# Kernel tuning notes

Hardware: AMD Instinct MI355X
Metric: run time of the kernel (lower is better)

Reference implementation:

```python
import jax, jax.numpy as jnp
import numpy as np

# Static architecture constants (match init_kwargs)
N, M, DIM = 2048, 4096, 256
KS = (0.9, 0.8, 0.7)
HEADS, BOT_HEADS = 4, 2
NEG_SLOPE = 0.2  # PyG GATConv default leaky-relu slope


def _p(key, shape, scale):
    return (scale * jax.random.normal(key, shape, dtype=jnp.float32))


def setup_inputs() -> dict:
    key = jax.random.key(0)
    ks = jax.random.split(key, 16)
    # Symmetric positive connectivity matrix (fMRI-like), fully dense
    R = jax.random.uniform(ks[0], (N, N), dtype=jnp.float32)
    A = 0.5 * (R + R.T)
    X = jax.random.normal(ks[1], (N, DIM), dtype=jnp.float32)
    s = 1.0 / np.sqrt(DIM).astype(np.float32)
    C, Cb = DIM // HEADS, DIM // BOT_HEADS
    inp = {
        'A': A, 'X': X,
        'W_down': _p(ks[2], (3, DIM, DIM), s),
        'as_down': _p(ks[3], (3, HEADS, C), s),
        'ad_down': _p(ks[4], (3, HEADS, C), s),
        'b_down': jnp.zeros((3, DIM), jnp.float32),
        'W_up': _p(ks[5], (3, DIM, DIM), s),
        'as_up': _p(ks[6], (3, HEADS, C), s),
        'ad_up': _p(ks[7], (3, HEADS, C), s),
        'b_up': jnp.zeros((3, DIM), jnp.float32),
        'W_bot': _p(ks[8], (DIM, DIM), s),
        'as_bot': _p(ks[9], (BOT_HEADS, Cb), s),
        'ad_bot': _p(ks[10], (BOT_HEADS, Cb), s),
        'b_bot': jnp.zeros((DIM,), jnp.float32),
        'W_pool': _p(ks[11], (3, DIM), s),
        'b_pool': jnp.zeros((3,), jnp.float32),
        'W_ups': _p(ks[12], (M, N), 1.0 / np.sqrt(N).astype(np.float32)),
        'b_ups': jnp.zeros((M,), jnp.float32),
    }
    return inp


def _sym_norm(A):
    # A_tilde = A + I ; D^{-1/2} A_tilde D^{-1/2} as elementwise broadcast
    A = A + jnp.eye(A.shape[0], dtype=A.dtype)
    d = A.sum(axis=1) + 1e-5
    di = d ** -0.5
    return di[:, None] * A * di[None, :]


def _gat(A, X, W, a_src, a_dst, b):
    # Dense-masked GATConv (concat=True, eval mode => no dropout).
    # Edge j->i exists iff A[j, i] > 0 (dense_to_sparse row=src, col=tgt).
    n = X.shape[0]
    H, C = a_src.shape
    x = (X @ W).reshape(n, H, C)                       # [n, H, C]
    s = jnp.einsum('nhc,hc->nh', x, a_src)             # source logit term
    t = jnp.einsum('nhc,hc->nh', x, a_dst)             # target logit term
    logits = jax.nn.leaky_relu(t[:, None, :] + s[None, :, :], NEG_SLOPE)  # [i, j, h]
    mask = (A.T > 0)[:, :, None]
    attn = jax.nn.softmax(jnp.where(mask, logits, -jnp.inf), axis=1)
    out = jnp.einsum('ijh,jhc->ihc', attn, x).reshape(n, H * C) + b
    return jax.nn.relu(out)


def reference(A, X, W_down, as_down, ad_down, b_down,
              W_up, as_up, ad_up, b_up,
              W_bot, as_bot, ad_bot, b_bot,
              W_pool, b_pool, W_ups, b_ups):
    A = _sym_norm(A)
    A_hist, idx_hist = [], []
    # Encoder: GAT -> top-k pool (gather rows/cols)
    for i in range(3):
        X = _gat(A, X, W_down[i], as_down[i], ad_down[i], b_down[i])
        A_hist.append(A)
        scores = jax.nn.sigmoid(X @ W_pool[i] + b_pool[i])
        k = max(2, int(KS[i] * A.shape[0]))            # static sizes
        vals, idx = jax.lax.top_k(scores, k)
        X = X[idx] * vals[:, None]
        A = A[idx][:, idx]
        idx_hist.append(idx)
    X = _gat(A, X, W_bot, as_bot, ad_bot, b_bot)
    # Decoder: scatter-unpool -> GAT -> adjacency reconstruction
    for i in range(3):
        u = 2 - i
        A, idx = A_hist[u], idx_hist[u]
        Xn = jnp.zeros((A.shape[0], X.shape[1]), X.dtype).at[idx].set(X)
        X = _gat(A, Xn, W_up[i], as_up[i], ad_up[i], b_up[i])
    # Upsampler: Linear(n->m) on X^T, then A_up = relu(Xu Xu^T)
    X_up = W_ups @ X + b_ups[:, None]                  # [M, DIM]
    A_up = jax.nn.relu(X_up @ X_up.T)                  # [M, M]
    return A_up
```

## Files before the change

kernel.cpp:

```cpp
#include <hip/hip_runtime.h>
#include <math.h>

#define NEG 0.2f
#define NMAX 2048
#define CHUNK 64
#define NCHMAX 32

__device__ __forceinline__ float lrelu(float v) { return v > 0.f ? v : NEG * v; }
__device__ __forceinline__ unsigned fenc(float v) {
    unsigned u = __float_as_uint(v);
    return (u & 0x80000000u) ? ~u : (u | 0x80000000u);
}
__device__ __forceinline__ float fdec(unsigned u) {
    return (u & 0x80000000u) ? __uint_as_float(u ^ 0x80000000u) : __uint_as_float(~u);
}

__global__ __launch_bounds__(256) void gemm_ks(const float* __restrict__ A,
                                               const float* __restrict__ B,
                                               float* __restrict__ C, int M, int N, int K) {
    __shared__ float As[16][68];
    __shared__ float Bs[16][68];
    const int tid = threadIdx.x;
    const int m0 = blockIdx.x * 64, n0 = blockIdx.y * 64;
    const int kchunk = K / gridDim.z;
    const int kbeg = blockIdx.z * kchunk, kend = kbeg + kchunk;
    const int tm = tid >> 4, tn = tid & 15;
    const int lr = tid >> 2, lc4 = (tid & 3) * 4;
    const int br = tid >> 4, bc4 = (tid & 15) * 4;
    float acc[4][4] = {{0.f}};
    for (int k0 = kbeg; k0 < kend; k0 += 16) {
        {
            int m = m0 + lr;
            float4 v = make_float4(0.f, 0.f, 0.f, 0.f);
            if (m < M) v = *(const float4*)(A + (size_t)m * K + k0 + lc4);
            As[lc4 + 0][lr] = v.x; As[lc4 + 1][lr] = v.y;
            As[lc4 + 2][lr] = v.z; As[lc4 + 3][lr] = v.w;
        }
        {
            float4 v = *(const float4*)(B + (size_t)(k0 + br) * N + n0 + bc4);
            *(float4*)&Bs[br][bc4] = v;
        }
        __syncthreads();
#pragma unroll
        for (int kk = 0; kk < 16; ++kk) {
            float a[4], b[4];
            *(float4*)a = *(const float4*)&As[kk][tm * 4];
            *(float4*)b = *(const float4*)&Bs[kk][tn * 4];
#pragma unroll
            for (int x = 0; x < 4; ++x)
#pragma unroll
                for (int y = 0; y < 4; ++y) acc[x][y] = fmaf(a[x], b[y], acc[x][y]);
        }
        __syncthreads();
    }
#pragma unroll
    for (int x = 0; x < 4; ++x) {
        int m = m0 + tm * 4 + x;
        if (m >= M) continue;
        float* dst = C + (size_t)m * N + n0 + tn * 4;
#pragma unroll
        for (int y = 0; y < 4; ++y) atomicAdd(dst + y, acc[x][y]);
    }
}

__global__ __launch_bounds__(256) void st_kernel(const float* __restrict__ xw,
                                                 const float* __restrict__ asrc,
                                                 const float* __restrict__ adst,
                                                 float* __restrict__ S, float* __restrict__ T,
                                                 unsigned* __restrict__ SMX,
                                                 int n, int Hh, int Cc) {
    int gid = blockIdx.x * 256 + threadIdx.x;
    int i = gid / Hh, h = gid - i * Hh;
    float s = -INFINITY;
    if (i < n) {
        const float* xr = xw + (size_t)i * 256 + h * Cc;
        const float* pa = asrc + h * Cc;
        const float* pd = adst + h * Cc;
        float sv = 0.f, tv = 0.f;
        for (int c = 0; c < Cc; c += 4) {
            float4 xv = *(const float4*)(xr + c);
            float4 av = *(const float4*)(pa + c);
            float4 dv = *(const float4*)(pd + c);
            sv += xv.x * av.x + xv.y * av.y + xv.z * av.z + xv.w * av.w;
            tv += xv.x * dv.x + xv.y * dv.y + xv.z * dv.z + xv.w * dv.w;
        }
        S[(size_t)i * Hh + h] = sv;
        T[(size_t)i * Hh + h] = tv;
        s = sv;
    }
    for (int off = Hh; off < 64; off <<= 1) s = fmaxf(s, __shfl_xor(s, off));
    int lane = threadIdx.x & 63;
    if (lane < Hh && s > -INFINITY) atomicMax(SMX + lane, fenc(s));
}

__global__ __launch_bounds__(256) void rank_k(const float* __restrict__ S,
                                              float* __restrict__ SS, int* __restrict__ PERM,
                                              int n, int Hh) {
    __shared__ float s[NMAX];
    int h = blockIdx.y;
    for (int j = threadIdx.x; j < n; j += 256) s[j] = S[(size_t)j * Hh + h];
    __syncthreads();
    int i = blockIdx.x * 256 + threadIdx.x;
    if (i >= n) return;
    float v = s[i];
    int cnt = 0, j = 0;
    for (; j + 4 <= n; j += 4) {
        float4 sv = *(const float4*)&s[j];
        cnt += (sv.x > v) || (sv.x == v && (j + 0) < i);
        cnt += (sv.y > v) || (sv.y == v && (j + 1) < i);
        cnt += (sv.z > v) || (sv.z == v && (j + 2) < i);
        cnt += (sv.w > v) || (sv.w == v && (j + 3) < i);
    }
    for (; j < n; ++j) {
        float sj = s[j];
        cnt += (sj > v) || (sj == v && j < i);
    }
    SS[h * NMAX + cnt] = v;
    PERM[h * NMAX + cnt] = i;
}

__global__ void scanA(const float* __restrict__ XW, const float* __restrict__ SS,
                      const int* __restrict__ PERM, const unsigned* __restrict__ SMX,
                      float* __restrict__ P1L, float* __restrict__ S2L,
                      float* __restrict__ Z1L, float* __restrict__ Z2L,
                      float* __restrict__ TOT1, float* __restrict__ TOT2,
                      float* __restrict__ ZT1, float* __restrict__ ZT2, int n) {
    const int C = blockDim.x, c = threadIdx.x;
    const int h = blockIdx.x, dir = blockIdx.y, ch = blockIdx.z;
    const float smax = fdec(SMX[h]);
    const int r0 = ch * CHUNK, r1 = min(n, r0 + CHUNK);
    float carry = 0.f, zc = 0.f;
    if (dir == 0) {
#pragma unroll 4
        for (int r = r0; r < r1; ++r) {
            float ssv = SS[h * NMAX + r];
            int j = PERM[h * NMAX + r];
            float xv = XW[(size_t)j * 256 + h * C + c];
            P1L[((size_t)h * NMAX + r) * C + c] = carry;
            if (c == 0) Z1L[h * NMAX + r] = zc;
            float w = expf(ssv - smax);
            carry = fmaf(w, xv, carry);
            zc += w;
        }
        TOT1[((size_t)h * NCHMAX + ch) * C + c] = carry;
        if (c == 0) ZT1[h * NCHMAX + ch] = zc;
    } else {
#pragma unroll 4
        for (int r = r1 - 1; r >= r0; --r) {
            float ssv = SS[h * NMAX + r];
            int j = PERM[h * NMAX + r];
            float xv = XW[(size_t)j * 256 + h * C + c];
            float w = expf(NEG * (ssv - smax));
            carry = fmaf(w, xv, carry);
            zc += w;
            S2L[((size_t)h * NMAX + r) * C + c] = carry;
            if (c == 0) Z2L[h * NMAX + r] = zc;
        }
        TOT2[((size_t)h * NCHMAX + ch) * C + c] = carry;
        if (c == 0) ZT2[h * NCHMAX + ch] = zc;
    }
}

__global__ void scanB(const float* __restrict__ TOT1, const float* __restrict__ TOT2,
                      const float* __restrict__ ZT1, const float* __restrict__ ZT2,
                      float* __restrict__ OFF1, float* __restrict__ OFFB,
                      float* __restrict__ ZO1, float* __restrict__ ZOB, int nch) {
    const int C = blockDim.x, c = threadIdx.x;
    const int h = blockIdx.x, dir = blockIdx.y;
    if (dir == 0) {
        float off = 0.f, zo = 0.f;
        for (int ch = 0; ch <= nch; ++ch) {
            OFF1[((size_t)h * (NCHMAX + 1) + ch) * C + c] = off;
            if (c == 0) ZO1[h * (NCHMAX + 1) + ch] = zo;
            if (ch < nch) {
                off += TOT1[((size_t)h * NCHMAX + ch) * C + c];
                if (c == 0) {}
                zo += ZT1[h * NCHMAX + ch];
            }
        }
    } else {
        float off = 0.f, zo = 0.f;
        for (int ch = nch - 1; ch >= 0; --ch) {
            OFFB[((size_t)h * (NCHMAX + 1) + ch) * C + c] = off;
            if (c == 0) ZOB[h * (NCHMAX + 1) + ch] = zo;
            off += TOT2[((size_t)h * NCHMAX + ch) * C + c];
            zo += ZT2[h * NCHMAX + ch];
        }
    }
}

__global__ __launch_bounds__(256) void combine_k(
    const float* __restrict__ P1L, const float* __restrict__ S2L,
    const float* __restrict__ Z1L, const float* __restrict__ Z2L,
    const float* __restrict__ OFF1, const float* __restrict__ OFFB,
    const float* __restrict__ ZO1, const float* __restrict__ ZOB,
    const float* __restrict__ SS, const float* __restrict__ T,
    const unsigned* __restrict__ SMX, const float* __restrict__ bias,
    const float* __restrict__ Wp, const float* __restrict__ bp,
    float* __restrict__ Xout, float* __restrict__ SC, int n, int Hh) {
    const int i = blockIdx.x, t = threadIdx.x;
    const int C = 256 / Hh;
    const int nch = (n + CHUNK - 1) / CHUNK;
    __shared__ int qs[4];
    __shared__ float f1s[4], f2s[4], invs[4];
    __shared__ float red[256];
    if (t < Hh) {
        int h = t;
        float tv = T[(size_t)i * Hh + h];
        float smax = fdec(SMX[h]);
        float u = tv + smax, m = lrelu(u);
        float f1 = expf(u - m), f2 = expf(NEG * u - m);
        float thr = -tv;
        int lo = 0, hi = n;
        while (lo < hi) {
            int mid = (lo + hi) >> 1;
            if (SS[h * NMAX + mid] > thr) lo = mid + 1; else hi = mid;
        }
        int q = lo;
        float z1, z2;
        if (q == n) {
            z1 = ZO1[h * (NCHMAX + 1) + nch];
            z2 = 0.f;
        } else {
            int ch = q / CHUNK;
            z1 = ZO1[h * (NCHMAX + 1) + ch] + Z1L[h * NMAX + q];
            z2 = ZOB[h * (NCHMAX + 1) + ch] + Z2L[h * NMAX + q];
        }
        qs[h] = q; f1s[h] = f1; f2s[h] = f2;
        invs[h] = 1.f / (f1 * z1 + f2 * z2);
    }
    __syncthreads();
    const int h = t / C, c = t - h * C;
    const int q = qs[h];
    const float f1 = f1s[h], f2 = f2s[h], inv = invs[h];
    float p1, s2;
    if (q == n) {
        p1 = OFF1[((size_t)h * (NCHMAX + 1) + nch) * C + c];
        s2 = 0.f;
    } else {
        int ch = q / CHUNK;
        p1 = OFF1[((size_t)h * (NCHMAX + 1) + ch) * C + c] + P1L[((size_t)h * NMAX + q) * C + c];
        s2 = OFFB[((size_t)h * (NCHMAX + 1) + ch) * C + c] + S2L[((size_t)h * NMAX + q) * C + c];
    }
    float out = fmaf(f1, p1, f2 * s2) * inv + bias[t];
    out = fmaxf(out, 0.f);
    Xout[(size_t)i * 256 + t] = out;
    if (Wp) {
        red[t] = out * Wp[t];
        __syncthreads();
        for (int s = 128; s > 0; s >>= 1) {
            if (t < s) red[t] += red[t + s];
            __syncthreads();
        }
        if (t == 0) SC[i] = 1.f / (1.f + expf(-(red[0] + bp[0])));
    }
}

__global__ __launch_bounds__(256) void topk_k(const float* __restrict__ SC,
                                              int* __restrict__ IDX, int n, int k) {
    __shared__ float s[NMAX];
    for (int j = threadIdx.x; j < n; j += 256) s[j] = SC[j];
    __syncthreads();
    int i = blockIdx.x * 256 + threadIdx.x;
    if (i >= n) return;
    float v = s[i];
    int cnt = 0, j = 0;
    for (; j + 4 <= n; j += 4) {
        float4 sv = *(const float4*)&s[j];
        cnt += (sv.x > v) || (sv.x == v && (j + 0) < i);
        cnt += (sv.y > v) || (sv.y == v && (j + 1) < i);
        cnt += (sv.z > v) || (sv.z == v && (j + 2) < i);
        cnt += (sv.w > v) || (sv.w == v && (j + 3) < i);
    }
    for (; j < n; ++j) {
        float sj = s[j];
        cnt += (sj > v) || (sj == v && j < i);
    }
    if (cnt < k) IDX[cnt] = i;
}

__global__ __launch_bounds__(256) void gather_k(const float* __restrict__ Xin,
                                                const float* __restrict__ SC,
                                                const int* __restrict__ IDX,
                                                float* __restrict__ Xout, int k) {
    int gid = blockIdx.x * 256 + threadIdx.x;
    if (gid >= k * 64) return;
    int r = gid >> 6, d4 = (gid & 63) * 4;
    int src = IDX[r];
    float val = SC[src];
    float4 x = *(const float4*)(Xin + (size_t)src * 256 + d4);
    x.x *= val; x.y *= val; x.z *= val; x.w *= val;
    *(float4*)(Xout + (size_t)r * 256 + d4) = x;
}

__global__ __launch_bounds__(256) void scatter_k(const float* __restrict__ Xin,
                                                 const int* __restrict__ IDX,
                                                 float* __restrict__ Xout, int k) {
    int gid = blockIdx.x * 256 + threadIdx.x;
    if (gid >= k * 64) return;
    int r = gid >> 6, d4 = (gid & 63) * 4;
    int dst = IDX[r];
    *(float4*)(Xout + (size_t)dst * 256 + d4) = *(const float4*)(Xin + (size_t)r * 256 + d4);
}

__global__ __launch_bounds__(256) void ttr_sym(const float* __restrict__ A,
                                               const float* __restrict__ bias,
                                               float* __restrict__ C, int M, int K) {
    if (blockIdx.y < blockIdx.x) return;
    __shared__ float As[8][132];
    __shared__ float Bs[8][132];
    const int tid = threadIdx.x;
    const int m0 = blockIdx.x * 128, n0 = blockIdx.y * 128;
    const int lr = tid >> 1, lc4 = (tid & 1) * 4;
    const int tm = tid >> 4, tn = tid & 15;
    const float abias = bias[m0 + lr], bbias = bias[n0 + lr];
    float acc[8][8] = {{0.f}};
    for (int k0 = 0; k0 < K; k0 += 8) {
        float4 va = *(const float4*)(A + (size_t)(m0 + lr) * K + k0 + lc4);
        float4 vb = *(const float4*)(A + (size_t)(n0 + lr) * K + k0 + lc4);
        va.x += abias; va.y += abias; va.z += abias; va.w += abias;
        vb.x += bbias; vb.y += bbias; vb.z += bbias; vb.w += bbias;
        As[lc4 + 0][lr] = va.x; As[lc4 + 1][lr] = va.y;
        As[lc4 + 2][lr] = va.z; As[lc4 + 3][lr] = va.w;
        Bs[lc4 + 0][lr] = vb.x; Bs[lc4 + 1][lr] = vb.y;
        Bs[lc4 + 2][lr] = vb.z; Bs[lc4 + 3][lr] = vb.w;
        __syncthreads();
#pragma unroll
        for (int kk = 0; kk < 8; ++kk) {
            float a[8], b[8];
            *(float4*)&a[0] = *(const float4*)&As[kk][tm * 8];
            *(float4*)&a[4] = *(const float4*)&As[kk][tm * 8 + 4];
            *(float4*)&b[0] = *(const float4*)&Bs[kk][tn * 8];
            *(float4*)&b[4] = *(const float4*)&Bs[kk][tn * 8 + 4];
#pragma unroll
            for (int x = 0; x < 8; ++x)
#pragma unroll
                for (int y = 0; y < 8; ++y) acc[x][y] = fmaf(a[x], b[y], acc[x][y]);
        }
        __syncthreads();
    }
#pragma unroll
    for (int x = 0; x < 8; ++x)
#pragma unroll
        for (int y = 0; y < 8; ++y) acc[x][y] = fmaxf(acc[x][y], 0.f);
#pragma unroll
    for (int x = 0; x < 8; ++x) {
        float* dst = C + (size_t)(m0 + tm * 8 + x) * M + n0 + tn * 8;
        *(float4*)dst = make_float4(acc[x][0], acc[x][1], acc[x][2], acc[x][3]);
        *(float4*)(dst + 4) = make_float4(acc[x][4], acc[x][5], acc[x][6], acc[x][7]);
    }
    if (blockIdx.x != blockIdx.y) {
#pragma unroll
        for (int y = 0; y < 8; ++y) {
            float* dst = C + (size_t)(n0 + tn * 8 + y) * M + m0 + tm * 8;
            *(float4*)dst = make_float4(acc[0][y], acc[1][y], acc[2][y], acc[3][y]);
            *(float4*)(dst + 4) = make_float4(acc[4][y], acc[5][y], acc[6][y], acc[7][y]);
        }
    }
}

extern "C" void kernel_launch(void* const* d_in, const int* in_sizes, int n_in,
                              void* d_out, int out_size, void* d_ws, size_t ws_size,
                              hipStream_t stream) {
    const float* X0      = (const float*)d_in[1];
    const float* W_down  = (const float*)d_in[2];
    const float* as_down = (const float*)d_in[3];
    const float* ad_down = (const float*)d_in[4];
    const float* b_down  = (const float*)d_in[5];
    const float* W_up    = (const float*)d_in[6];
    const float* as_up   = (const float*)d_in[7];
    const float* ad_up   = (const float*)d_in[8];
    const float* b_up    = (const float*)d_in[9];
    const float* W_bot   = (const float*)d_in[10];
    const float* as_bot  = (const float*)d_in[11];
    const float* ad_bot  = (const float*)d_in[12];
    const float* b_bot   = (const float*)d_in[13];
    const float* W_pool  = (const float*)d_in[14];
    const float* b_pool  = (const float*)d_in[15];
    const float* W_ups   = (const float*)d_in[16];
    const float* b_ups   = (const float*)d_in[17];
    float* out = (float*)d_out;

    float* F = (float*)d_ws;
    size_t o = 0;
    float* Xa  = F + o; o += 2048 * 256;
    float* Xb  = F + o; o += 2048 * 256;
    float* XW  = F + o; o += 2048 * 256;
    unsigned* SMX = (unsigned*)(F + o); o += 16;
    float* S   = F + o; o += 2048 * 4;
    float* T   = F + o; o += 2048 * 4;
    float* SS  = F + o; o += 2048 * 4;
    int* PERM  = (int*)(F + o); o += 2048 * 4;
    float* Z1L = F + o; o += 2048 * 4;
    float* Z2L = F + o; o += 2048 * 4;
    float* TOT1 = F + o; o += 8192;
    float* TOT2 = F + o; o += 8192;
    float* OFF1 = F + o; o += 8448;
    float* OFFB = F + o; o += 8448;
    float* ZT1 = F + o; o += 128;
    float* ZT2 = F + o; o += 128;
    float* ZO1 = F + o; o += 136;
    float* ZOB = F + o; o += 136;
    float* SC  = F + o; o += 2048;
    int* IDXs[3];
    IDXs[0] = (int*)(F + o); o += 2048;
    IDXs[1] = (int*)(F + o); o += 2048;
    IDXs[2] = (int*)(F + o); o += 2048;
    float* P1L = F + o; o += 2048 * 256;
    float* S2L = F + o; o += 2048 * 256;
    float* XU  = P1L;

    auto cdiv = [](int a, int b) { return (a + b - 1) / b; };

    auto run_gat = [&](const float* Xin, float* Xout, int n, const float* W,
                       const float* asrc, const float* adst, const float* bias, int Hh,
                       const float* Wp, const float* bp) {
        int C = 256 / Hh;
        int nch = cdiv(n, CHUNK);
        hipMemsetAsync(XW, 0, (size_t)(2048 * 256 + 16) * 4, stream);
        gemm_ks<<<dim3(cdiv(n, 64), 4, 2), 256, 0, stream>>>(Xin, W, XW, n, 256, 256);
        st_kernel<<<cdiv(n * Hh, 256), 256, 0, stream>>>(XW, asrc, adst, S, T, SMX, n, Hh, C);
        rank_k<<<dim3(cdiv(n, 256), Hh), 256, 0, stream>>>(S, SS, PERM, n, Hh);
        scanA<<<dim3(Hh, 2, nch), C, 0, stream>>>(XW, SS, PERM, SMX, P1L, S2L, Z1L, Z2L,
                                                  TOT1, TOT2, ZT1, ZT2, n);
        scanB<<<dim3(Hh, 2), C, 0, stream>>>(TOT1, TOT2, ZT1, ZT2, OFF1, OFFB, ZO1, ZOB, nch);
        combine_k<<<n, 256, 0, stream>>>(P1L, S2L, Z1L, Z2L, OFF1, OFFB, ZO1, ZOB, SS, T,
                                         SMX, bias, Wp, bp, Xout, SC, n, Hh);
    };

    const int ns[4] = {2048, 1843, 1474, 1031};

    const float* cur = X0;
    for (int l = 0; l < 3; ++l) {
        int n = ns[l], k = ns[l + 1];
        run_gat(cur, Xb, n, W_down + (size_t)l * 65536, as_down + l * 256, ad_down + l * 256,
                b_down + l * 256, 4, W_pool + l * 256, b_pool + l);
        topk_k<<<cdiv(n, 256), 256, 0, stream>>>(SC, IDXs[l], n, k);
        gather_k<<<cdiv(k * 64, 256), 256, 0, stream>>>(Xb, SC, IDXs[l], Xa, k);
        cur = Xa;
    }

    run_gat(Xa, Xb, ns[3], W_bot, as_bot, ad_bot, b_bot, 2, nullptr, nullptr);

    for (int i = 0; i < 3; ++i) {
        int u = 2 - i;
        int pn = ns[u], kc = ns[u + 1];
        hipMemsetAsync(Xa, 0, (size_t)pn * 256 * 4, stream);
        scatter_k<<<cdiv(kc * 64, 256), 256, 0, stream>>>(Xb, IDXs[u], Xa, kc);
        run_gat(Xa, Xb, pn, W_up + (size_t)i * 65536, as_up + i * 256, ad_up + i * 256,
                b_up + i * 256, 4, nullptr, nullptr);
    }

    hipMemsetAsync(XU, 0, (size_t)4096 * 256 * 4, stream);
    gemm_ks<<<dim3(64, 4, 4), 256, 0, stream>>>(W_ups, Xb, XU, 4096, 256, 2048);
    ttr_sym<<<dim3(32, 32), 256, 0, stream>>>(XU, b_ups, out, 4096, 256);
}
```

Baseline: 1.229 ms.

## Fuse gather/scatter into GEMM, replace scan with chunk totals, retile symmetric output

New measurement: 1.183 ms. -3.8%, faster.

```diff
diff --git a/kernel.cpp b/kernel.cpp
--- a/kernel.cpp
+++ b/kernel.cpp
@@ -17,7 +17,11 @@
 
 __global__ __launch_bounds__(256) void gemm_ks(const float* __restrict__ A,
                                                const float* __restrict__ B,
-                                               float* __restrict__ C, int M, int N, int K) {
+                                               float* __restrict__ C,
+                                               const int* __restrict__ rowmapA,
+                                               const float* __restrict__ rowscale,
+                                               const int* __restrict__ rowmapC,
+                                               int M, int N, int K) {
     __shared__ float As[16][68];
     __shared__ float Bs[16][68];
     const int tid = threadIdx.x;
@@ -27,20 +31,24 @@
     const int tm = tid >> 4, tn = tid & 15;
     const int lr = tid >> 2, lc4 = (tid & 3) * 4;
     const int br = tid >> 4, bc4 = (tid & 15) * 4;
+    const int am = m0 + lr;
+    const bool aval = am < M;
+    int arow = 0; float ascale = 1.f;
+    if (aval) { arow = rowmapA ? rowmapA[am] : am; if (rowscale) ascale = rowscale[arow]; }
+    const float* Ap = A + (size_t)arow * K;
+    float4 va = make_float4(0.f, 0.f, 0.f, 0.f), vb;
+    if (aval) va = *(const float4*)(Ap + kbeg + lc4);
+    vb = *(const float4*)(B + (size_t)(kbeg + br) * N + n0 + bc4);
     float acc[4][4] = {{0.f}};
     for (int k0 = kbeg; k0 < kend; k0 += 16) {
-        {
-            int m = m0 + lr;
-            float4 v = make_float4(0.f, 0.f, 0.f, 0.f);
-            if (m < M) v = *(const float4*)(A + (size_t)m * K + k0 + lc4);
-            As[lc4 + 0][lr] = v.x; As[lc4 + 1][lr] = v.y;
-            As[lc4 + 2][lr] = v.z; As[lc4 + 3][lr] = v.w;
-        }
-        {
-            float4 v = *(const float4*)(B + (size_t)(k0 + br) * N + n0 + bc4);
-            *(float4*)&Bs[br][bc4] = v;
-        }
+        As[lc4 + 0][lr] = va.x * ascale; As[lc4 + 1][lr] = va.y * ascale;
+        As[lc4 + 2][lr] = va.z * ascale; As[lc4 + 3][lr] = va.w * ascale;
+        *(float4*)&Bs[br][bc4] = vb;
         __syncthreads();
+        if (k0 + 16 < kend) {
+            if (aval) va = *(const float4*)(Ap + k0 + 16 + lc4);
+            vb = *(const float4*)(B + (size_t)(k0 + 16 + br) * N + n0 + bc4);
+        }
 #pragma unroll
         for (int kk = 0; kk < 16; ++kk) {
             float a[4], b[4];
@@ -57,7 +65,8 @@
     for (int x = 0; x < 4; ++x) {
         int m = m0 + tm * 4 + x;
         if (m >= M) continue;
-        float* dst = C + (size_t)m * N + n0 + tn * 4;
+        int orow = rowmapC ? rowmapC[m] : m;
+        float* dst = C + (size_t)orow * N + n0 + tn * 4;
 #pragma unroll
         for (int y = 0; y < 4; ++y) atomicAdd(dst + y, acc[x][y]);
     }
@@ -119,97 +128,80 @@
     PERM[h * NMAX + cnt] = i;
 }
 
-__global__ void scanA(const float* __restrict__ XW, const float* __restrict__ SS,
-                      const int* __restrict__ PERM, const unsigned* __restrict__ SMX,
-                      float* __restrict__ P1L, float* __restrict__ S2L,
-                      float* __restrict__ Z1L, float* __restrict__ Z2L,
-                      float* __restrict__ TOT1, float* __restrict__ TOT2,
-                      float* __restrict__ ZT1, float* __restrict__ ZT2, int n) {
-    const int C = blockDim.x, c = threadIdx.x;
-    const int h = blockIdx.x, dir = blockIdx.y, ch = blockIdx.z;
+__global__ __launch_bounds__(256) void chunk_k(const float* __restrict__ XW,
+                                               const float* __restrict__ SS,
+                                               const int* __restrict__ PERM,
+                                               const unsigned* __restrict__ SMX,
+                                               float* __restrict__ TOT1, float* __restrict__ TOT2,
+                                               float* __restrict__ ZT1, float* __restrict__ ZT2,
+                                               int n, int Cc) {
+    const int h = blockIdx.x, ch = blockIdx.y;
+    const int nh = 256 / Cc, seg = CHUNK / nh;
+    const int c = threadIdx.x % Cc, half = threadIdx.x / Cc;
+    __shared__ float ssh[CHUNK];
+    __shared__ int pjh[CHUNK];
+    __shared__ float red1[256], red2[256];
+    __shared__ float zr1[4], zr2[4];
+    if (threadIdx.x < CHUNK) {
+        int rk = ch * CHUNK + threadIdx.x;
+        ssh[threadIdx.x] = (rk < n) ? SS[h * NMAX + rk] : 0.f;
+        pjh[threadIdx.x] = (rk < n) ? PERM[h * NMAX + rk] : -1;
+    }
+    __syncthreads();
     const float smax = fdec(SMX[h]);
-    const int r0 = ch * CHUNK, r1 = min(n, r0 + CHUNK);
-    float carry = 0.f, zc = 0.f;
-    if (dir == 0) {
+    float t1 = 0.f, t2 = 0.f, z1 = 0.f, z2 = 0.f;
 #pragma unroll 4
-        for (int r = r0; r < r1; ++r) {
-            float ssv = SS[h * NMAX + r];
-            int j = PERM[h * NMAX + r];
-            float xv = XW[(size_t)j * 256 + h * C + c];
-            P1L[((size_t)h * NMAX + r) * C + c] = carry;
-            if (c == 0) Z1L[h * NMAX + r] = zc;
-            float w = expf(ssv - smax);
-            carry = fmaf(w, xv, carry);
-            zc += w;
-        }
-        TOT1[((size_t)h * NCHMAX + ch) * C + c] = carry;
-        if (c == 0) ZT1[h * NCHMAX + ch] = zc;
-    } else {
-#pragma unroll 4
-        for (int r = r1 - 1; r >= r0; --r) {
-            float ssv = SS[h * NMAX + r];
-            int j = PERM[h * NMAX + r];
-            float xv = XW[(size_t)j * 256 + h * C + c];
-            float w = expf(NEG * (ssv - smax));
-            carry = fmaf(w, xv, carry);
-            zc += w;
-            S2L[((size_t)h * NMAX + r) * C + c] = carry;
-            if (c == 0) Z2L[h * NMAX + r] = zc;
-        }
-        TOT2[((size_t)h * NCHMAX + ch) * C + c] = carry;
-        if (c == 0) ZT2[h * NCHMAX + ch] = zc;
-    }
-}
-
-__global__ void scanB(const float* __restrict__ TOT1, const float* __restrict__ TOT2,
-                      const float* __restrict__ ZT1, const float* __restrict__ ZT2,
-                      float* __restrict__ OFF1, float* __restrict__ OFFB,
-                      float* __restrict__ ZO1, float* __restrict__ ZOB, int nch) {
-    const int C = blockDim.x, c = threadIdx.x;
-    const int h = blockIdx.x, dir = blockIdx.y;
-    if (dir == 0) {
-        float off = 0.f, zo = 0.f;
-        for (int ch = 0; ch <= nch; ++ch) {
-            OFF1[((size_t)h * (NCHMAX + 1) + ch) * C + c] = off;
-            if (c == 0) ZO1[h * (NCHMAX + 1) + ch] = zo;
-            if (ch < nch) {
-                off += TOT1[((size_t)h * NCHMAX + ch) * C + c];
-                if (c == 0) {}
-                zo += ZT1[h * NCHMAX + ch];
-            }
-        }
-    } else {
-        float off = 0.f, zo = 0.f;
-        for (int ch = nch - 1; ch >= 0; --ch) {
-            OFFB[((size_t)h * (NCHMAX + 1) + ch) * C + c] = off;
-            if (c == 0) ZOB[h * (NCHMAX + 1) + ch] = zo;
-            off += TOT2[((size_t)h * NCHMAX + ch) * C + c];
-            zo += ZT2[h * NCHMAX + ch];
+    for (int q = 0; q < seg; ++q) {
+        int r = half * seg + q;
+        int j = pjh[r];
+        if (j < 0) continue;
+        float d = ssh[r] - smax;
+        float w1 = expf(d), w2 = expf(NEG * d);
+        float x = XW[(size_t)j * 256 + h * Cc + c];
+        t1 = fmaf(w1, x, t1); t2 = fmaf(w2, x, t2);
+        z1 += w1; z2 += w2;
+    }
+    red1[threadIdx.x] = t1; red2[threadIdx.x] = t2;
+    if (c == 0) { zr1[half] = z1; zr2[half] = z2; }
+    __syncthreads();
+    if (half == 0) {
+        for (int hh = 1; hh < nh; ++hh) { t1 += red1[hh * Cc + c]; t2 += red2[hh * Cc + c]; }
+        TOT1[((size_t)h * NCHMAX + ch) * Cc + c] = t1;
+        TOT2[((size_t)h * NCHMAX + ch) * Cc + c] = t2;
+        if (c == 0) {
+            float a = z1, b = z2;
+            for (int hh = 1; hh < nh; ++hh) { a += zr1[hh]; b += zr2[hh]; }
+            ZT1[h * NCHMAX + ch] = a;
+            ZT2[h * NCHMAX + ch] = b;
         }
     }
 }
 
 __global__ __launch_bounds__(256) void combine_k(
-    const float* __restrict__ P1L, const float* __restrict__ S2L,
-    const float* __restrict__ Z1L, const float* __restrict__ Z2L,
-    const float* __restrict__ OFF1, const float* __restrict__ OFFB,
-    const float* __restrict__ ZO1, const float* __restrict__ ZOB,
-    const float* __restrict__ SS, const float* __restrict__ T,
-    const unsigned* __restrict__ SMX, const float* __restrict__ bias,
-    const float* __restrict__ Wp, const float* __restrict__ bp,
-    float* __restrict__ Xout, float* __restrict__ SC, int n, int Hh) {
+    const float* __restrict__ XW, const float* __restrict__ SS,
+    const int* __restrict__ PERM, const unsigned* __restrict__ SMX,
+    const float* __restrict__ T,
+    const float* __restrict__ TOT1, const float* __restrict__ TOT2,
+    const float* __restrict__ ZT1, const float* __restrict__ ZT2,
+    const float* __restrict__ bias, const float* __restrict__ Wp,
+    const float* __restrict__ bp,
+    float* __restrict__ Xout, float* __restrict__ SC, int n, int Hh, int nch) {
     const int i = blockIdx.x, t = threadIdx.x;
     const int C = 256 / Hh;
-    const int nch = (n + CHUNK - 1) / CHUNK;
-    __shared__ int qs[4];
-    __shared__ float f1s[4], f2s[4], invs[4];
-    __shared__ float red[256];
+    __shared__ float f1s[4], f2s[4], invs[4], smaxs[4];
+    __shared__ int qs[4], chs[4];
+    __shared__ float coef[256];
+    __shared__ int permsh[256];
+    __shared__ float redw[4];
+    float z1p = 0.f, z2s = 0.f;
     if (t < Hh) {
         int h = t;
+        float smax = fdec(SMX[h]);
+        smaxs[h] = smax;
         float tv = T[(size_t)i * Hh + h];
-        float smax = fdec(SMX[h]);
         float u = tv + smax, m = lrelu(u);
-        float f1 = expf(u - m), f2 = expf(NEG * u - m);
+        f1s[h] = expf(u - m);
+        f2s[h] = expf(NEG * u - m);
         float thr = -tv;
         int lo = 0, hi = n;
         while (lo < hi) {
@@ -217,42 +209,53 @@
             if (SS[h * NMAX + mid] > thr) lo = mid + 1; else hi = mid;
         }
         int q = lo;
-        float z1, z2;
-        if (q == n) {
-            z1 = ZO1[h * (NCHMAX + 1) + nch];
-            z2 = 0.f;
-        } else {
-            int ch = q / CHUNK;
-            z1 = ZO1[h * (NCHMAX + 1) + ch] + Z1L[h * NMAX + q];
-            z2 = ZOB[h * (NCHMAX + 1) + ch] + Z2L[h * NMAX + q];
-        }
-        qs[h] = q; f1s[h] = f1; f2s[h] = f2;
-        invs[h] = 1.f / (f1 * z1 + f2 * z2);
+        int ch = min(q / CHUNK, nch - 1);
+        qs[h] = q; chs[h] = ch;
+        for (int cc = 0; cc < ch; ++cc) z1p += ZT1[h * NCHMAX + cc];
+        for (int cc = ch + 1; cc < nch; ++cc) z2s += ZT2[h * NCHMAX + cc];
+    }
+    __syncthreads();
+    if (t < Hh * CHUNK) {
+        int h = t >> 6, r = t & 63;
+        int rank = chs[h] * CHUNK + r;
+        float w = 0.f; int j = 0;
+        if (rank < n) {
+            float ssv = SS[h * NMAX + rank];
+            j = PERM[h * NMAX + rank];
+            float d = ssv - smaxs[h];
+            w = (rank < qs[h]) ? f1s[h] * expf(d) : f2s[h] * expf(NEG * d);
+        }
+        coef[t] = w; permsh[t] = j;
+    }
+    __syncthreads();
+    if (t < Hh) {
+        int h = t;
+        float den = fmaf(f1s[h], z1p, f2s[h] * z2s);
+        for (int r = 0; r < CHUNK; ++r) den += coef[h * CHUNK + r];
+        invs[h] = 1.f / den;
     }
     __syncthreads();
     const int h = t / C, c = t - h * C;
-    const int q = qs[h];
-    const float f1 = f1s[h], f2 = f2s[h], inv = invs[h];
-    float p1, s2;
-    if (q == n) {
-        p1 = OFF1[((size_t)h * (NCHMAX + 1) + nch) * C + c];
-        s2 = 0.f;
-    } else {
-        int ch = q / CHUNK;
-        p1 = OFF1[((size_t)h * (NCHMAX + 1) + ch) * C + c] + P1L[((size_t)h * NMAX + q) * C + c];
-        s2 = OFFB[((size_t)h * (NCHMAX + 1) + ch) * C + c] + S2L[((size_t)h * NMAX + q) * C + c];
-    }
-    float out = fmaf(f1, p1, f2 * s2) * inv + bias[t];
+    const float* xcol = XW + h * C + c;
+    float csum = 0.f;
+#pragma unroll 8
+    for (int r = 0; r < CHUNK; ++r)
+        csum = fmaf(coef[h * CHUNK + r], xcol[(size_t)permsh[h * CHUNK + r] * 256], csum);
+    float a1 = 0.f, a2 = 0.f;
+    const int ch = chs[h];
+    for (int cc = 0; cc < ch; ++cc) a1 += TOT1[((size_t)h * NCHMAX + cc) * C + c];
+    for (int cc = ch + 1; cc < nch; ++cc) a2 += TOT2[((size_t)h * NCHMAX + cc) * C + c];
+    float out = (fmaf(f1s[h], a1, f2s[h] * a2) + csum) * invs[h] + bias[t];
     out = fmaxf(out, 0.f);
     Xout[(size_t)i * 256 + t] = out;
     if (Wp) {
-        red[t] = out * Wp[t];
+        float v = out * Wp[t];
+#pragma unroll
+        for (int off = 32; off; off >>= 1) v += __shfl_xor(v, off);
+        if ((t & 63) == 0) redw[t >> 6] = v;
         __syncthreads();
-        for (int s = 128; s > 0; s >>= 1) {
-            if (t < s) red[t] += red[t + s];
-            __syncthreads();
-        }
-        if (t == 0) SC[i] = 1.f / (1.f + expf(-(red[0] + bp[0])));
+        if (t == 0)
+            SC[i] = 1.f / (1.f + expf(-(redw[0] + redw[1] + redw[2] + redw[3] + bp[0])));
     }
 }
 
@@ -279,59 +282,47 @@
     if (cnt < k) IDX[cnt] = i;
 }
 
-__global__ __launch_bounds__(256) void gather_k(const float* __restrict__ Xin,
-                                                const float* __restrict__ SC,
-                                                const int* __restrict__ IDX,
-                                                float* __restrict__ Xout, int k) {
-    int gid = blockIdx.x * 256 + threadIdx.x;
-    if (gid >= k * 64) return;
-    int r = gid >> 6, d4 = (gid & 63) * 4;
-    int src = IDX[r];
-    float val = SC[src];
-    float4 x = *(const float4*)(Xin + (size_t)src * 256 + d4);
-    x.x *= val; x.y *= val; x.z *= val; x.w *= val;
-    *(float4*)(Xout + (size_t)r * 256 + d4) = x;
-}
-
-__global__ __launch_bounds__(256) void scatter_k(const float* __restrict__ Xin,
-                                                 const int* __restrict__ IDX,
-                                                 float* __restrict__ Xout, int k) {
-    int gid = blockIdx.x * 256 + threadIdx.x;
-    if (gid >= k * 64) return;
-    int r = gid >> 6, d4 = (gid & 63) * 4;
-    int dst = IDX[r];
-    *(float4*)(Xout + (size_t)dst * 256 + d4) = *(const float4*)(Xin + (size_t)r * 256 + d4);
-}
-
 __global__ __launch_bounds__(256) void ttr_sym(const float* __restrict__ A,
                                                const float* __restrict__ bias,
                                                float* __restrict__ C, int M, int K) {
-    if (blockIdx.y < blockIdx.x) return;
-    __shared__ float As[8][132];
-    __shared__ float Bs[8][132];
+    const int L = blockIdx.x;
+    int by = (int)((sqrtf(8.f * L + 1.f) - 1.f) * 0.5f);
+    while ((by + 1) * (by + 2) / 2 <= L) ++by;
+    while (by * (by + 1) / 2 > L) --by;
+    const int bx = L - by * (by + 1) / 2;
+    __shared__ float As[16][132];
+    __shared__ float Bs[16][132];
     const int tid = threadIdx.x;
-    const int m0 = blockIdx.x * 128, n0 = blockIdx.y * 128;
-    const int lr = tid >> 1, lc4 = (tid & 1) * 4;
+    const int m0 = bx * 128, n0 = by * 128;
+    const int lr = tid >> 1, lc8 = (tid & 1) * 8;
     const int tm = tid >> 4, tn = tid & 15;
-    const float abias = bias[m0 + lr], bbias = bias[n0 + lr];
+    const float ab = bias[m0 + lr], bb = bias[n0 + lr];
+    const float* Ar = A + (size_t)(m0 + lr) * K;
+    const float* Br = A + (size_t)(n0 + lr) * K;
+    float4 va0 = *(const float4*)(Ar + lc8), va1 = *(const float4*)(Ar + lc8 + 4);
+    float4 vb0 = *(const float4*)(Br + lc8), vb1 = *(const float4*)(Br + lc8 + 4);
     float acc[8][8] = {{0.f}};
-    for (int k0 = 0; k0 < K; k0 += 8) {
-        float4 va = *(const float4*)(A + (size_t)(m0 + lr) * K + k0 + lc4);
-        float4 vb = *(const float4*)(A + (size_t)(n0 + lr) * K + k0 + lc4);
-        va.x += abias; va.y += abias; va.z += abias; va.w += abias;
-        vb.x += bbias; vb.y += bbias; vb.z += bbias; vb.w += bbias;
-        As[lc4 + 0][lr] = va.x; As[lc4 + 1][lr] = va.y;
-        As[lc4 + 2][lr] = va.z; As[lc4 + 3][lr] = va.w;
-        Bs[lc4 + 0][lr] = vb.x; Bs[lc4 + 1][lr] = vb.y;
-        Bs[lc4 + 2][lr] = vb.z; Bs[lc4 + 3][lr] = vb.w;
+    for (int k0 = 0; k0 < K; k0 += 16) {
+        As[lc8 + 0][lr] = va0.x + ab; As[lc8 + 1][lr] = va0.y + ab;
+        As[lc8 + 2][lr] = va0.z + ab; As[lc8 + 3][lr] = va0.w + ab;
+        As[lc8 + 4][lr] = va1.x + ab; As[lc8 + 5][lr] = va1.y + ab;
+        As[lc8 + 6][lr] = va1.z + ab; As[lc8 + 7][lr] = va1.w + ab;
+        Bs[lc8 + 0][lr] = vb0.x + bb; Bs[lc8 + 1][lr] = vb0.y + bb;
+        Bs[lc8 + 2][lr] = vb0.z + bb; Bs[lc8 + 3][lr] = vb0.w + bb;
+        Bs[lc8 + 4][lr] = vb1.x + bb; Bs[lc8 + 5][lr] = vb1.y + bb;
+        Bs[lc8 + 6][lr] = vb1.z + bb; Bs[lc8 + 7][lr] = vb1.w + bb;
         __syncthreads();
-#pragma unroll
-        for (int kk = 0; kk < 8; ++kk) {
+        if (k0 + 16 < K) {
+            va0 = *(const float4*)(Ar + k0 + 16 + lc8); va1 = *(const float4*)(Ar + k0 + 20 + lc8);
+            vb0 = *(const float4*)(Br + k0 + 16 + lc8); vb1 = *(const float4*)(Br + k0 + 20 + lc8);
+        }
+#pragma unroll
+        for (int kk = 0; kk < 16; ++kk) {
             float a[8], b[8];
-            *(float4*)&a[0] = *(const float4*)&As[kk][tm * 8];
-            *(float4*)&a[4] = *(const float4*)&As[kk][tm * 8 + 4];
-            *(float4*)&b[0] = *(const float4*)&Bs[kk][tn * 8];
-            *(float4*)&b[4] = *(const float4*)&Bs[kk][tn * 8 + 4];
+            *(float4*)&a[0] = *(const float4*)&As[kk][tm * 4];
+            *(float4*)&a[4] = *(const float4*)&As[kk][64 + tm * 4];
+            *(float4*)&b[0] = *(const float4*)&Bs[kk][tn * 4];
+            *(float4*)&b[4] = *(const float4*)&Bs[kk][64 + tn * 4];
 #pragma unroll
             for (int x = 0; x < 8; ++x)
 #pragma unroll
@@ -345,16 +336,18 @@
         for (int y = 0; y < 8; ++y) acc[x][y] = fmaxf(acc[x][y], 0.f);
 #pragma unroll
     for (int x = 0; x < 8; ++x) {
-        float* dst = C + (size_t)(m0 + tm * 8 + x) * M + n0 + tn * 8;
-        *(float4*)dst = make_float4(acc[x][0], acc[x][1], acc[x][2], acc[x][3]);
-        *(float4*)(dst + 4) = make_float4(acc[x][4], acc[x][5], acc[x][6], acc[x][7]);
-    }
-    if (blockIdx.x != blockIdx.y) {
+        int row = m0 + ((x < 4) ? tm * 4 + x : 64 + tm * 4 + (x - 4));
+        float* dst = C + (size_t)row * M + n0;
+        *(float4*)(dst + tn * 4) = make_float4(acc[x][0], acc[x][1], acc[x][2], acc[x][3]);
+        *(float4*)(dst + 64 + tn * 4) = make_float4(acc[x][4], acc[x][5], acc[x][6], acc[x][7]);
+    }
+    if (bx != by) {
 #pragma unroll
         for (int y = 0; y < 8; ++y) {
-            float* dst = C + (size_t)(n0 + tn * 8 + y) * M + m0 + tm * 8;
-            *(float4*)dst = make_float4(acc[0][y], acc[1][y], acc[2][y], acc[3][y]);
-            *(float4*)(dst + 4) = make_float4(acc[4][y], acc[5][y], acc[6][y], acc[7][y]);
+            int row = n0 + ((y < 4) ? tn * 4 + y : 64 + tn * 4 + (y - 4));
+            float* dst = C + (size_t)row * M + m0;
+            *(float4*)(dst + tm * 4) = make_float4(acc[0][y], acc[1][y], acc[2][y], acc[3][y]);
+            *(float4*)(dst + 64 + tm * 4) = make_float4(acc[4][y], acc[5][y], acc[6][y], acc[7][y]);
         }
     }
 }
@@ -383,7 +376,6 @@
 
     float* F = (float*)d_ws;
     size_t o = 0;
-    float* Xa  = F + o; o += 2048 * 256;
     float* Xb  = F + o; o += 2048 * 256;
     float* XW  = F + o; o += 2048 * 256;
     unsigned* SMX = (unsigned*)(F + o); o += 16;
@@ -391,67 +383,59 @@
     float* T   = F + o; o += 2048 * 4;
     float* SS  = F + o; o += 2048 * 4;
     int* PERM  = (int*)(F + o); o += 2048 * 4;
-    float* Z1L = F + o; o += 2048 * 4;
-    float* Z2L = F + o; o += 2048 * 4;
     float* TOT1 = F + o; o += 8192;
     float* TOT2 = F + o; o += 8192;
-    float* OFF1 = F + o; o += 8448;
-    float* OFFB = F + o; o += 8448;
     float* ZT1 = F + o; o += 128;
     float* ZT2 = F + o; o += 128;
-    float* ZO1 = F + o; o += 136;
-    float* ZOB = F + o; o += 136;
     float* SC  = F + o; o += 2048;
     int* IDXs[3];
     IDXs[0] = (int*)(F + o); o += 2048;
     IDXs[1] = (int*)(F + o); o += 2048;
     IDXs[2] = (int*)(F + o); o += 2048;
-    float* P1L = F + o; o += 2048 * 256;
-    float* S2L = F + o; o += 2048 * 256;
-    float* XU  = P1L;
+    float* XU  = F + o; o += 4096 * 256;
 
     auto cdiv = [](int a, int b) { return (a + b - 1) / b; };
 
-    auto run_gat = [&](const float* Xin, float* Xout, int n, const float* W,
+    auto run_gat = [&](const float* Xin, int Mrows, int n, const float* W,
                        const float* asrc, const float* adst, const float* bias, int Hh,
+                       const int* rmA, const float* rscale, const int* rmC,
                        const float* Wp, const float* bp) {
         int C = 256 / Hh;
         int nch = cdiv(n, CHUNK);
         hipMemsetAsync(XW, 0, (size_t)(2048 * 256 + 16) * 4, stream);
-        gemm_ks<<<dim3(cdiv(n, 64), 4, 2), 256, 0, stream>>>(Xin, W, XW, n, 256, 256);
+        gemm_ks<<<dim3(cdiv(Mrows, 64), 4, 4), 256, 0, stream>>>(Xin, W, XW, rmA, rscale,
+                                                                 rmC, Mrows, 256, 256);
         st_kernel<<<cdiv(n * Hh, 256), 256, 0, stream>>>(XW, asrc, adst, S, T, SMX, n, Hh, C);
         rank_k<<<dim3(cdiv(n, 256), Hh), 256, 0, stream>>>(S, SS, PERM, n, Hh);
-        scanA<<<dim3(Hh, 2, nch), C, 0, stream>>>(XW, SS, PERM, SMX, P1L, S2L, Z1L, Z2L,
-                                                  TOT1, TOT2, ZT1, ZT2, n);
-        scanB<<<dim3(Hh, 2), C, 0, stream>>>(TOT1, TOT2, ZT1, ZT2, OFF1, OFFB, ZO1, ZOB, nch);
-        combine_k<<<n, 256, 0, stream>>>(P1L, S2L, Z1L, Z2L, OFF1, OFFB, ZO1, ZOB, SS, T,
-                                         SMX, bias, Wp, bp, Xout, SC, n, Hh);
+        chunk_k<<<dim3(Hh, nch), 256, 0, stream>>>(XW, SS, PERM, SMX, TOT1, TOT2, ZT1, ZT2,
+                                                   n, C);
+        combine_k<<<n, 256, 0, stream>>>(XW, SS, PERM, SMX, T, TOT1, TOT2, ZT1, ZT2, bias,
+                                         Wp, bp, Xb, SC, n, Hh, nch);
     };
 
     const int ns[4] = {2048, 1843, 1474, 1031};
 
-    const float* cur = X0;
     for (int l = 0; l < 3; ++l) {
         int n = ns[l], k = ns[l + 1];
-        run_gat(cur, Xb, n, W_down + (size_t)l * 65536, as_down + l * 256, ad_down + l * 256,
-                b_down + l * 256, 4, W_pool + l * 256, b_pool + l);
+        run_gat(l ? Xb : X0, n, n, W_down + (size_t)l * 65536, as_down + l * 256,
+                ad_down + l * 256, b_down + l * 256, 4,
+                l ? IDXs[l - 1] : nullptr, l ? SC : nullptr, nullptr,
+                W_pool + l * 256, b_pool + l);
         topk_k<<<cdiv(n, 256), 256, 0, stream>>>(SC, IDXs[l], n, k);
-        gather_k<<<cdiv(k * 64, 256), 256, 0, stream>>>(Xb, SC, IDXs[l], Xa, k);
-        cur = Xa;
-    }
-
-    run_gat(Xa, Xb, ns[3], W_bot, as_bot, ad_bot, b_bot, 2, nullptr, nullptr);
+    }
+
+    run_gat(Xb, ns[3], ns[3], W_bot, as_bot, ad_bot, b_bot, 2, IDXs[2], SC, nullptr,
+            nullptr, nullptr);
 
     for (int i = 0; i < 3; ++i) {
         int u = 2 - i;
         int pn = ns[u], kc = ns[u + 1];
-        hipMemsetAsync(Xa, 0, (size_t)pn * 256 * 4, stream);
-        scatter_k<<<cdiv(kc * 64, 256), 256, 0, stream>>>(Xb, IDXs[u], Xa, kc);
-        run_gat(Xa, Xb, pn, W_up + (size_t)i * 65536, as_up + i * 256, ad_up + i * 256,
-                b_up + i * 256, 4, nullptr, nullptr);
+        run_gat(Xb, kc, pn, W_up + (size_t)i * 65536, as_up + i * 256, ad_up + i * 256,
+                b_up + i * 256, 4, nullptr, nullptr, IDXs[u], nullptr, nullptr);
     }
 
     hipMemsetAsync(XU, 0, (size_t)4096 * 256 * 4, stream);
-    gemm_ks<<<dim3(64, 4, 4), 256, 0, stream>>>(W_ups, Xb, XU, 4096, 256, 2048);
-    ttr_sym<<<dim3(32, 32), 256, 0, stream>>>(XU, b_ups, out, 4096, 256);
-}
+    gemm_ks<<<dim3(64, 4, 4), 256, 0, stream>>>(W_ups, Xb, XU, nullptr, nullptr, nullptr,
+                                                4096, 256, 2048);
+    ttr_sym<<<528, 256, 0, stream>>>(XU, b_ups, out, 4096, 256);
+}
```
